# Kernel tuning notes

Measured on AMD Instinct MI355X. Metric: run time of the kernel, lower is better.

Reference implementation:

```python
import jax, jax.numpy as jnp
import numpy as np

HIDDEN_DIM = 4096
NUM_EXPERTS = 64
TOP_K = 8
ROUTED_SCALING_FACTOR = 2.5
NUM_TOKENS = 16384


def setup_inputs() -> dict:
    key = jax.random.key(0)
    kx, kw = jax.random.split(key)
    x = jax.random.normal(kx, (NUM_TOKENS, HIDDEN_DIM), dtype=jnp.float32)
    # gate Linear weight (no bias): torch Linear stores [out, in]; we keep [in, out] for x @ W
    W = jax.random.normal(kw, (HIDDEN_DIM, NUM_EXPERTS), dtype=jnp.float32) * (1.0 / np.sqrt(HIDDEN_DIM))
    e_score_correction_bias = jnp.zeros((NUM_EXPERTS,), dtype=jnp.float32)
    return {"x": x, "W": W, "e_score_correction_bias": e_score_correction_bias}


def reference(x, W, e_score_correction_bias):
    # logits: [T, E]
    logits = jnp.einsum("td,de->te", x, W)
    scores = jax.nn.sigmoid(logits)
    scores_with_bias = scores + e_score_correction_bias
    # top-k over experts (sorted descending, matches torch.topk sorted=True)
    _, topk_indices = jax.lax.top_k(scores_with_bias, TOP_K)  # [T, k]
    # gather the UNBIASED scores at the selected experts
    topk_scores = jnp.take_along_axis(scores, topk_indices, axis=-1)  # [T, k]
    scores_sum = jnp.sum(topk_scores, axis=-1, keepdims=True) + 1e-20
    topk_weights = topk_scores / scores_sum * ROUTED_SCALING_FACTOR
    return topk_indices, topk_weights
```

## Files before the change

### kernel.cpp

```cpp
#include <hip/hip_runtime.h>
#include <math.h>

#define NT 16384
#define HD 4096
#define NE 64
#define TT 64
#define DC 64
#define SX 66
#define SL 65
#define NCH (HD / DC)

__device__ __forceinline__ double dsig(double z) { return 1.0 / (1.0 + exp(-z)); }

__global__ __launch_bounds__(256) void moe_gate(const float* __restrict__ X,
                                                const float* __restrict__ Wg,
                                                const float* __restrict__ bias,
                                                float* __restrict__ out) {
    __shared__ double sX[DC][SX];
    __shared__ double sW[DC][NE];
    __shared__ double sL[TT][SL];
    __shared__ double sB[NE];

    const int tid   = threadIdx.x;
    const int tok0  = blockIdx.x * TT;
    const int tr    = tid >> 4;
    const int tc    = tid & 15;
    const int tok_s = tid >> 2;
    const int dv    = tid & 3;

    if (tid < NE) sB[tid] = (double)bias[tid];

    double acc[4][4];
#pragma unroll
    for (int i = 0; i < 4; ++i)
#pragma unroll
        for (int j = 0; j < 4; ++j) acc[i][j] = 0.0;

    const float* xrow = X + (size_t)(tok0 + tok_s) * HD;

    float4 xr[4], wr[4];
#pragma unroll
    for (int s = 0; s < 4; ++s) {
        xr[s] = *(const float4*)(xrow + s * 16 + dv * 4);
        wr[s] = *(const float4*)(Wg + (size_t)(tid + 256 * s) * 4);
    }

    for (int k = 0; k < NCH; ++k) {
        __syncthreads();
#pragma unroll
        for (int s = 0; s < 4; ++s) {
            const int dl = s * 16 + dv * 4;
            sX[dl + 0][tok_s] = (double)xr[s].x;
            sX[dl + 1][tok_s] = (double)xr[s].y;
            sX[dl + 2][tok_s] = (double)xr[s].z;
            sX[dl + 3][tok_s] = (double)xr[s].w;
            const int f = (tid + 256 * s) * 4;
            const int d = f >> 6, e = f & 63;
            sW[d][e + 0] = (double)wr[s].x;
            sW[d][e + 1] = (double)wr[s].y;
            sW[d][e + 2] = (double)wr[s].z;
            sW[d][e + 3] = (double)wr[s].w;
        }
        __syncthreads();
        if (k + 1 < NCH) {
            const float* xp = xrow + (k + 1) * DC;
            const float* wp = Wg + (size_t)(k + 1) * DC * NE;
#pragma unroll
            for (int s = 0; s < 4; ++s) {
                xr[s] = *(const float4*)(xp + s * 16 + dv * 4);
                wr[s] = *(const float4*)(wp + (size_t)(tid + 256 * s) * 4);
            }
        }
#pragma unroll
        for (int dd = 0; dd < DC; ++dd) {
            const double2 xa = *(const double2*)&sX[dd][tr * 4];
            const double2 xb = *(const double2*)&sX[dd][tr * 4 + 2];
            const double2 wa = *(const double2*)&sW[dd][tc * 2];
            const double2 wb = *(const double2*)&sW[dd][tc * 2 + 32];
            acc[0][0] += xa.x * wa.x; acc[0][1] += xa.x * wa.y;
            acc[0][2] += xa.x * wb.x; acc[0][3] += xa.x * wb.y;
            acc[1][0] += xa.y * wa.x; acc[1][1] += xa.y * wa.y;
            acc[1][2] += xa.y * wb.x; acc[1][3] += xa.y * wb.y;
            acc[2][0] += xb.x * wa.x; acc[2][1] += xb.x * wa.y;
            acc[2][2] += xb.x * wb.x; acc[2][3] += xb.x * wb.y;
            acc[3][0] += xb.y * wa.x; acc[3][1] += xb.y * wa.y;
            acc[3][2] += xb.y * wb.x; acc[3][3] += xb.y * wb.y;
        }
    }

    __syncthreads();
    const int e0 = tc * 2, e2 = tc * 2 + 32;
#pragma unroll
    for (int i = 0; i < 4; ++i) {
        const int t = tr * 4 + i;
        sL[t][e0 + 0] = dsig(acc[i][0]);
        sL[t][e0 + 1] = dsig(acc[i][1]);
        sL[t][e2 + 0] = dsig(acc[i][2]);
        sL[t][e2 + 1] = dsig(acc[i][3]);
    }
    __syncthreads();

    if (tid < TT) {
        const int t = tid;
        double bsc[8];
        int    bix[8];
#pragma unroll
        for (int r = 0; r < 8; ++r) { bsc[r] = -INFINITY; bix[r] = 0; }
        for (int e = 0; e < NE; ++e) {
            double cb = sL[t][e] + sB[e];
            int    ci = e;
#pragma unroll
            for (int r = 0; r < 8; ++r) {
                const bool sw = cb > bsc[r];
                const double tb = bsc[r]; const int ti = bix[r];
                bsc[r] = sw ? cb : tb;  bix[r] = sw ? ci : ti;
                cb     = sw ? tb : cb;  ci     = sw ? ti : ci;
            }
        }
        double us[8];
        double sum = 1e-20;
#pragma unroll
        for (int r = 0; r < 8; ++r) { us[r] = sL[t][bix[r]]; sum += us[r]; }

        const size_t o = (size_t)(tok0 + t) * 8;
        float4 i0 = {(float)bix[0], (float)bix[1], (float)bix[2], (float)bix[3]};
        float4 i1 = {(float)bix[4], (float)bix[5], (float)bix[6], (float)bix[7]};
        *(float4*)(out + o)     = i0;
        *(float4*)(out + o + 4) = i1;
        float* ow = out + (size_t)NT * 8;
        const double sc = 2.5 / sum;
        float4 w0 = {(float)(us[0] * sc), (float)(us[1] * sc),
                     (float)(us[2] * sc), (float)(us[3] * sc)};
        float4 w1 = {(float)(us[4] * sc), (float)(us[5] * sc),
                     (float)(us[6] * sc), (float)(us[7] * sc)};
        *(float4*)(ow + o)     = w0;
        *(float4*)(ow + o + 4) = w1;
    }
}

extern "C" void kernel_launch(void* const* d_in, const int* in_sizes, int n_in,
                              void* d_out, int out_size, void* d_ws, size_t ws_size,
                              hipStream_t stream) {
    const float* X  = (const float*)d_in[0];
    const float* Wg = (const float*)d_in[1];
    const float* b  = (const float*)d_in[2];
    float* out = (float*)d_out;
    dim3 grid(NT / TT), block(256);
    hipLaunchKernelGGL(moe_gate, grid, block, 0, stream, X, Wg, b, out);
}
```

Before: 568.9 us.

## Compute gate in fp32 and recompute ambiguous tokens in fp64

```diff
diff --git a/kernel.cpp b/kernel.cpp
--- a/kernel.cpp
+++ b/kernel.cpp
@@ -4,147 +4,229 @@
 #define NT 16384
 #define HD 4096
 #define NE 64
-#define TT 64
+#define TT 32
 #define DC 64
-#define SX 66
-#define SL 65
 #define NCH (HD / DC)
-
+#define SXS 34
+#define SLS 65
+#define GAP_THRESH 4e-5f
+
+__device__ __forceinline__ float fsig(float z) { return 1.0f / (1.0f + expf(-z)); }
 __device__ __forceinline__ double dsig(double z) { return 1.0 / (1.0 + exp(-z)); }
 
-__global__ __launch_bounds__(256) void moe_gate(const float* __restrict__ X,
-                                                const float* __restrict__ Wg,
-                                                const float* __restrict__ bias,
-                                                float* __restrict__ out) {
-    __shared__ double sX[DC][SX];
-    __shared__ double sW[DC][NE];
-    __shared__ double sL[TT][SL];
-    __shared__ double sB[NE];
-
-    const int tid   = threadIdx.x;
-    const int tok0  = blockIdx.x * TT;
-    const int tr    = tid >> 4;
-    const int tc    = tid & 15;
-    const int tok_s = tid >> 2;
-    const int dv    = tid & 3;
-
-    if (tid < NE) sB[tid] = (double)bias[tid];
-
-    double acc[4][4];
+__global__ __launch_bounds__(256) void moe_gate_f32(
+    const float* __restrict__ X, const float* __restrict__ Wg,
+    const float* __restrict__ bias, float* __restrict__ out,
+    unsigned int* __restrict__ nflag, int* __restrict__ flags) {
+  __shared__ float sX[DC][SXS];
+  __shared__ float sW[DC][NE];
+  __shared__ float sL[TT][SLS];
+  __shared__ float sB[NE];
+
+  const int tid   = threadIdx.x;
+  const int tok0  = blockIdx.x * TT;
+  const int tr    = tid >> 4;
+  const int tc    = tid & 15;
+  const int tok_s = tid >> 3;
+  const int dv    = tid & 7;
+
+  if (tid < NE) sB[tid] = bias[tid];
+
+  float acc[2][4];
+#pragma unroll
+  for (int i = 0; i < 2; ++i)
+#pragma unroll
+    for (int j = 0; j < 4; ++j) acc[i][j] = 0.0f;
+
+  const float* xrow = X + (size_t)(tok0 + tok_s) * HD + dv * 8;
+
+  float4 xr[2], wr[4];
+#pragma unroll
+  for (int s = 0; s < 2; ++s) xr[s] = *(const float4*)(xrow + s * 4);
+#pragma unroll
+  for (int s = 0; s < 4; ++s)
+    wr[s] = *(const float4*)(Wg + (size_t)(tid + 256 * s) * 4);
+
+  for (int k = 0; k < NCH; ++k) {
+    __syncthreads();
+#pragma unroll
+    for (int s = 0; s < 2; ++s) {
+      const int d = dv * 8 + s * 4;
+      sX[d + 0][tok_s] = xr[s].x;
+      sX[d + 1][tok_s] = xr[s].y;
+      sX[d + 2][tok_s] = xr[s].z;
+      sX[d + 3][tok_s] = xr[s].w;
+    }
+#pragma unroll
+    for (int s = 0; s < 4; ++s) {
+      const int f = (tid + 256 * s) * 4;
+      *(float4*)&sW[f >> 6][f & 63] = wr[s];
+    }
+    __syncthreads();
+    if (k + 1 < NCH) {
+      const float* xp = xrow + (k + 1) * DC;
+      const float* wp = Wg + (size_t)(k + 1) * (DC * NE);
+#pragma unroll
+      for (int s = 0; s < 2; ++s) xr[s] = *(const float4*)(xp + s * 4);
+#pragma unroll
+      for (int s = 0; s < 4; ++s)
+        wr[s] = *(const float4*)(wp + (size_t)(tid + 256 * s) * 4);
+    }
+#pragma unroll
+    for (int dd = 0; dd < DC; ++dd) {
+      const float2 xa = *(const float2*)&sX[dd][tr * 2];
+      const float4 wa = *(const float4*)&sW[dd][tc * 4];
+      acc[0][0] += xa.x * wa.x; acc[0][1] += xa.x * wa.y;
+      acc[0][2] += xa.x * wa.z; acc[0][3] += xa.x * wa.w;
+      acc[1][0] += xa.y * wa.x; acc[1][1] += xa.y * wa.y;
+      acc[1][2] += xa.y * wa.z; acc[1][3] += xa.y * wa.w;
+    }
+  }
+
+  __syncthreads();
+#pragma unroll
+  for (int i = 0; i < 2; ++i) {
+    const int t = tr * 2 + i;
+    sL[t][tc * 4 + 0] = fsig(acc[i][0]);
+    sL[t][tc * 4 + 1] = fsig(acc[i][1]);
+    sL[t][tc * 4 + 2] = fsig(acc[i][2]);
+    sL[t][tc * 4 + 3] = fsig(acc[i][3]);
+  }
+  __syncthreads();
+
+  if (tid < TT) {
+    const int t = tid;
+    float bsc[9]; int bix[9];
+#pragma unroll
+    for (int r = 0; r < 9; ++r) { bsc[r] = -INFINITY; bix[r] = 0; }
+    for (int e = 0; e < NE; ++e) {
+      float cb = sL[t][e] + sB[e];
+      int   ci = e;
+#pragma unroll
+      for (int r = 0; r < 9; ++r) {
+        const bool sw = cb > bsc[r];
+        const float tb = bsc[r]; const int ti = bix[r];
+        bsc[r] = sw ? cb : tb;  bix[r] = sw ? ci : ti;
+        cb     = sw ? tb : cb;  ci     = sw ? ti : ci;
+      }
+    }
+    float mg = bsc[0] - bsc[1];
+#pragma unroll
+    for (int r = 1; r < 8; ++r) mg = fminf(mg, bsc[r] - bsc[r + 1]);
+
+    float us[8]; float sum = 1e-20f;
+#pragma unroll
+    for (int r = 0; r < 8; ++r) { us[r] = sL[t][bix[r]]; sum += us[r]; }
+    const float sc = 2.5f / sum;
+    const size_t o = (size_t)(tok0 + t) * 8;
+    float4 i0 = {(float)bix[0], (float)bix[1], (float)bix[2], (float)bix[3]};
+    float4 i1 = {(float)bix[4], (float)bix[5], (float)bix[6], (float)bix[7]};
+    *(float4*)(out + o)     = i0;
+    *(float4*)(out + o + 4) = i1;
+    float* ow = out + (size_t)NT * 8;
+    float4 w0 = {us[0] * sc, us[1] * sc, us[2] * sc, us[3] * sc};
+    float4 w1 = {us[4] * sc, us[5] * sc, us[6] * sc, us[7] * sc};
+    *(float4*)(ow + o)     = w0;
+    *(float4*)(ow + o + 4) = w1;
+
+    if (!(mg > GAP_THRESH)) {
+      const unsigned int p = atomicAdd(nflag, 1u);
+      if (p < NT) flags[p] = tok0 + t;
+    }
+  }
+}
+
+__global__ __launch_bounds__(256) void moe_gate_fix(
+    const float* __restrict__ X, const float* __restrict__ Wg,
+    const float* __restrict__ bias, float* __restrict__ out,
+    const unsigned int* __restrict__ nflag, const int* __restrict__ flags) {
+  __shared__ float  sx[HD];
+  __shared__ double sP[NE][9];
+  __shared__ double sS[NE];
+
+  const int tid = threadIdx.x;
+  unsigned int n = *nflag;
+  if (n > NT) n = NT;
+
+  for (unsigned int w = blockIdx.x; w < n; w += gridDim.x) {
+    const int t = flags[w];
+    __syncthreads();
+    const float4* xv = (const float4*)(X + (size_t)t * HD);
 #pragma unroll
     for (int i = 0; i < 4; ++i)
-#pragma unroll
-        for (int j = 0; j < 4; ++j) acc[i][j] = 0.0;
-
-    const float* xrow = X + (size_t)(tok0 + tok_s) * HD;
-
-    float4 xr[4], wr[4];
-#pragma unroll
-    for (int s = 0; s < 4; ++s) {
-        xr[s] = *(const float4*)(xrow + s * 16 + dv * 4);
-        wr[s] = *(const float4*)(Wg + (size_t)(tid + 256 * s) * 4);
-    }
-
-    for (int k = 0; k < NCH; ++k) {
-        __syncthreads();
-#pragma unroll
-        for (int s = 0; s < 4; ++s) {
-            const int dl = s * 16 + dv * 4;
-            sX[dl + 0][tok_s] = (double)xr[s].x;
-            sX[dl + 1][tok_s] = (double)xr[s].y;
-            sX[dl + 2][tok_s] = (double)xr[s].z;
-            sX[dl + 3][tok_s] = (double)xr[s].w;
-            const int f = (tid + 256 * s) * 4;
-            const int d = f >> 6, e = f & 63;
-            sW[d][e + 0] = (double)wr[s].x;
-            sW[d][e + 1] = (double)wr[s].y;
-            sW[d][e + 2] = (double)wr[s].z;
-            sW[d][e + 3] = (double)wr[s].w;
+      ((float4*)sx)[tid + 256 * i] = xv[tid + 256 * i];
+    __syncthreads();
+
+    const int ep = (tid & 31) * 2;
+    const int q  = tid >> 5;
+    const float* wp = Wg + (size_t)(q * 512) * NE + ep;
+    const float* xp = sx + q * 512;
+    double a0 = 0.0, a1 = 0.0, b0 = 0.0, b1 = 0.0;
+    for (int d = 0; d < 512; d += 2) {
+      const double x0 = (double)xp[d];
+      const double x1 = (double)xp[d + 1];
+      const float2 w0 = *(const float2*)(wp + (size_t)d * NE);
+      const float2 w1 = *(const float2*)(wp + (size_t)(d + 1) * NE);
+      a0 += x0 * (double)w0.x; a1 += x0 * (double)w0.y;
+      b0 += x1 * (double)w1.x; b1 += x1 * (double)w1.y;
+    }
+    sP[ep][q]     = a0 + b0;
+    sP[ep + 1][q] = a1 + b1;
+    __syncthreads();
+    if (tid < NE) {
+      double s = 0.0;
+#pragma unroll
+      for (int q8 = 0; q8 < 8; ++q8) s += sP[tid][q8];
+      sS[tid] = dsig(s);
+    }
+    __syncthreads();
+    if (tid == 0) {
+      double bsc[8]; int bix[8];
+#pragma unroll
+      for (int r = 0; r < 8; ++r) { bsc[r] = -INFINITY; bix[r] = 0; }
+      for (int e = 0; e < NE; ++e) {
+        double cb = sS[e] + (double)bias[e];
+        int   ci = e;
+#pragma unroll
+        for (int r = 0; r < 8; ++r) {
+          const bool sw = cb > bsc[r];
+          const double tb = bsc[r]; const int ti = bix[r];
+          bsc[r] = sw ? cb : tb;  bix[r] = sw ? ci : ti;
+          cb     = sw ? tb : cb;  ci     = sw ? ti : ci;
         }
-        __syncthreads();
-        if (k + 1 < NCH) {
-            const float* xp = xrow + (k + 1) * DC;
-            const float* wp = Wg + (size_t)(k + 1) * DC * NE;
-#pragma unroll
-            for (int s = 0; s < 4; ++s) {
-                xr[s] = *(const float4*)(xp + s * 16 + dv * 4);
-                wr[s] = *(const float4*)(wp + (size_t)(tid + 256 * s) * 4);
-            }
-        }
-#pragma unroll
-        for (int dd = 0; dd < DC; ++dd) {
-            const double2 xa = *(const double2*)&sX[dd][tr * 4];
-            const double2 xb = *(const double2*)&sX[dd][tr * 4 + 2];
-            const double2 wa = *(const double2*)&sW[dd][tc * 2];
-            const double2 wb = *(const double2*)&sW[dd][tc * 2 + 32];
-            acc[0][0] += xa.x * wa.x; acc[0][1] += xa.x * wa.y;
-            acc[0][2] += xa.x * wb.x; acc[0][3] += xa.x * wb.y;
-            acc[1][0] += xa.y * wa.x; acc[1][1] += xa.y * wa.y;
-            acc[1][2] += xa.y * wb.x; acc[1][3] += xa.y * wb.y;
-            acc[2][0] += xb.x * wa.x; acc[2][1] += xb.x * wa.y;
-            acc[2][2] += xb.x * wb.x; acc[2][3] += xb.x * wb.y;
-            acc[3][0] += xb.y * wa.x; acc[3][1] += xb.y * wa.y;
-            acc[3][2] += xb.y * wb.x; acc[3][3] += xb.y * wb.y;
-        }
-    }
-
-    __syncthreads();
-    const int e0 = tc * 2, e2 = tc * 2 + 32;
-#pragma unroll
-    for (int i = 0; i < 4; ++i) {
-        const int t = tr * 4 + i;
-        sL[t][e0 + 0] = dsig(acc[i][0]);
-        sL[t][e0 + 1] = dsig(acc[i][1]);
-        sL[t][e2 + 0] = dsig(acc[i][2]);
-        sL[t][e2 + 1] = dsig(acc[i][3]);
-    }
-    __syncthreads();
-
-    if (tid < TT) {
-        const int t = tid;
-        double bsc[8];
-        int    bix[8];
-#pragma unroll
-        for (int r = 0; r < 8; ++r) { bsc[r] = -INFINITY; bix[r] = 0; }
-        for (int e = 0; e < NE; ++e) {
-            double cb = sL[t][e] + sB[e];
-            int    ci = e;
-#pragma unroll
-            for (int r = 0; r < 8; ++r) {
-                const bool sw = cb > bsc[r];
-                const double tb = bsc[r]; const int ti = bix[r];
-                bsc[r] = sw ? cb : tb;  bix[r] = sw ? ci : ti;
-                cb     = sw ? tb : cb;  ci     = sw ? ti : ci;
-            }
-        }
-        double us[8];
-        double sum = 1e-20;
-#pragma unroll
-        for (int r = 0; r < 8; ++r) { us[r] = sL[t][bix[r]]; sum += us[r]; }
-
-        const size_t o = (size_t)(tok0 + t) * 8;
-        float4 i0 = {(float)bix[0], (float)bix[1], (float)bix[2], (float)bix[3]};
-        float4 i1 = {(float)bix[4], (float)bix[5], (float)bix[6], (float)bix[7]};
-        *(float4*)(out + o)     = i0;
-        *(float4*)(out + o + 4) = i1;
-        float* ow = out + (size_t)NT * 8;
-        const double sc = 2.5 / sum;
-        float4 w0 = {(float)(us[0] * sc), (float)(us[1] * sc),
-                     (float)(us[2] * sc), (float)(us[3] * sc)};
-        float4 w1 = {(float)(us[4] * sc), (float)(us[5] * sc),
-                     (float)(us[6] * sc), (float)(us[7] * sc)};
-        *(float4*)(ow + o)     = w0;
-        *(float4*)(ow + o + 4) = w1;
-    }
+      }
+      double us[8]; double sum = 1e-20;
+#pragma unroll
+      for (int r = 0; r < 8; ++r) { us[r] = sS[bix[r]]; sum += us[r]; }
+      const double sc = 2.5 / sum;
+      const size_t o = (size_t)t * 8;
+      float4 i0 = {(float)bix[0], (float)bix[1], (float)bix[2], (float)bix[3]};
+      float4 i1 = {(float)bix[4], (float)bix[5], (float)bix[6], (float)bix[7]};
+      *(float4*)(out + o)     = i0;
+      *(float4*)(out + o + 4) = i1;
+      float* ow = out + (size_t)NT * 8;
+      float4 w0 = {(float)(us[0] * sc), (float)(us[1] * sc),
+                   (float)(us[2] * sc), (float)(us[3] * sc)};
+      float4 w1 = {(float)(us[4] * sc), (float)(us[5] * sc),
+                   (float)(us[6] * sc), (float)(us[7] * sc)};
+      *(float4*)(ow + o)     = w0;
+      *(float4*)(ow + o + 4) = w1;
+    }
+  }
 }
 
 extern "C" void kernel_launch(void* const* d_in, const int* in_sizes, int n_in,
                               void* d_out, int out_size, void* d_ws, size_t ws_size,
                               hipStream_t stream) {
-    const float* X  = (const float*)d_in[0];
-    const float* Wg = (const float*)d_in[1];
-    const float* b  = (const float*)d_in[2];
-    float* out = (float*)d_out;
-    dim3 grid(NT / TT), block(256);
-    hipLaunchKernelGGL(moe_gate, grid, block, 0, stream, X, Wg, b, out);
+  const float* X  = (const float*)d_in[0];
+  const float* Wg = (const float*)d_in[1];
+  const float* b  = (const float*)d_in[2];
+  float* out = (float*)d_out;
+  unsigned int* nflag = (unsigned int*)d_ws;
+  int* flags = (int*)((char*)d_ws + 64);
+  hipMemsetAsync(d_ws, 0, 64, stream);
+  hipLaunchKernelGGL(moe_gate_f32, dim3(NT / TT), dim3(256), 0, stream,
+                     X, Wg, b, out, nflag, flags);
+  hipLaunchKernelGGL(moe_gate_fix, dim3(256), dim3(256), 0, stream,
+                     X, Wg, b, out, nflag, flags);
 }
```

New measurement: 569.6 us. No clear change (+0.1%).
